# Optimization experiments

Measured on AMD Instinct MI355X. Metric: run time of the kernel, lower is better.

## Reference

```python
import math
import jax, jax.numpy as jnp
import numpy as np

NUM_EXPERTS = 64
HIDDEN = 2048
BATCH, SEQ = 8, 2048


def setup_inputs() -> dict:
    key = jax.random.key(0)
    k1, k2 = jax.random.split(key)
    hidden_states = jax.random.normal(k1, (BATCH, SEQ, HIDDEN), dtype=jnp.float32)
    classifier_weight = jax.random.normal(k2, (HIDDEN, NUM_EXPERTS), dtype=jnp.float32) * (1.0 / math.sqrt(HIDDEN))
    return {"hidden_states": hidden_states, "classifier_weight": classifier_weight}


def _route_tokens(router_logits):
    # router_logits: (tokens, experts). second_expert_policy='all',
    # normalize_router_prob_before_dropping=False, batch_prioritized_routing=True,
    # training mode -> capacity = 2*ceil(tokens/experts), no padding mask.
    n_tokens, n_experts = router_logits.shape
    router_probs = jax.nn.softmax(router_logits, axis=-1)  # router_dtype=float32

    top_1_idx = jnp.argmax(router_probs, axis=-1)
    top_1_mask = jax.nn.one_hot(top_1_idx, n_experts, dtype=router_probs.dtype)
    logits_except_top_1 = jnp.where(top_1_mask > 0, -jnp.inf, router_logits)
    top_2_idx = jnp.argmax(logits_except_top_1, axis=-1)
    top_2_mask = jax.nn.one_hot(top_2_idx, n_experts, dtype=router_probs.dtype)

    # batch-prioritized routing: sort tokens by -max prob, cumsum positions per expert
    importance = -jnp.max(router_probs, axis=-1)  # (tokens,)
    order = jnp.argsort(importance)
    inv_order = jnp.argsort(order)
    sorted_1 = top_1_mask[order]
    locations1 = ((jnp.cumsum(sorted_1, axis=0) - 1.0) * sorted_1)[inv_order]
    sorted_2 = top_2_mask[order]
    locations2 = ((jnp.cumsum(sorted_2, axis=0) - 1.0) * sorted_2)[inv_order]
    locations2 = locations2 + jnp.sum(top_1_mask, axis=0, keepdims=True)

    expert_capacity = 2 * math.ceil(n_tokens / n_experts)  # training path, expert_capacity=None
    top_1_mask = top_1_mask * (locations1 < expert_capacity).astype(top_1_mask.dtype)
    top_2_mask = top_2_mask * (locations2 < expert_capacity).astype(top_2_mask.dtype)

    # normalize AFTER dropping (normalize_router_prob_before_dropping=False)
    top_1_max_probs = jnp.sum(router_probs * top_1_mask, axis=-1)
    top_2_max_probs = jnp.sum(router_probs * top_2_mask, axis=-1)
    denom = jnp.clip(top_1_max_probs + top_2_max_probs, jnp.finfo(router_probs.dtype).eps, None)
    gates1 = (top_1_max_probs / denom)[:, None] * top_1_mask
    gates2 = (top_2_max_probs / denom)[:, None] * top_2_mask
    return top_1_mask, gates1 + gates2


def reference(hidden_states, classifier_weight):
    b, s, h = hidden_states.shape
    x = hidden_states.reshape(b * s, h)
    router_logits = x @ classifier_weight  # (tokens, experts), bias=False
    top_1_mask, router_probs = _route_tokens(router_logits)
    return top_1_mask, router_probs
```

## Files before the change

kernel.cpp:

```cpp
#include <hip/hip_runtime.h>
#include <math.h>

#define TOKENS      16384
#define HID         2048
#define EXPERTS     64
#define CAPSLOT     1024
#define CAP         512

__device__ __forceinline__ void fma8(float* a, float s, float4 w0, float4 w1) {
    a[0] = fmaf(s, w0.x, a[0]); a[1] = fmaf(s, w0.y, a[1]);
    a[2] = fmaf(s, w0.z, a[2]); a[3] = fmaf(s, w0.w, a[3]);
    a[4] = fmaf(s, w1.x, a[4]); a[5] = fmaf(s, w1.y, a[5]);
    a[6] = fmaf(s, w1.z, a[6]); a[7] = fmaf(s, w1.w, a[7]);
}

__global__ __launch_bounds__(256, 2) void k_partial16(
    const float* __restrict__ x, const float* __restrict__ W,
    float* __restrict__ partial, int* __restrict__ cnts)
{
    __shared__ float wl[128 * EXPERTS];

    const int tid = threadIdx.x;
    const int tb = blockIdx.x & 31;
    const int kc = blockIdx.x >> 5;
    const int k0 = kc * 128;

    if (blockIdx.x == 0) {
        for (int i = tid; i < 128 * 16; i += 256) cnts[i] = 0;
    }

    {
        const float4* src = (const float4*)(W + (size_t)k0 * EXPERTS);
        float4* dst = (float4*)wl;
        #pragma unroll
        for (int i = 0; i < 8; ++i)
            dst[i * 256 + tid] = src[i * 256 + tid];
    }
    __syncthreads();

    const int lane = tid & 63;
    const int wv   = tid >> 6;
    const int tg   = lane >> 3;
    const int eg   = lane & 7;
    const int tok0 = tb * 512 + wv * 128 + tg * 16;
    const float* xb = x + (size_t)tok0 * HID + k0;

    float acc[16][8];
    #pragma unroll
    for (int i = 0; i < 16; ++i)
        #pragma unroll
        for (int e = 0; e < 8; ++e) acc[i][e] = 0.f;

    #pragma unroll 1
    for (int k4 = 0; k4 < 128; k4 += 4) {
        float4 xv[16];
        #pragma unroll
        for (int i = 0; i < 16; ++i)
            xv[i] = *(const float4*)(xb + (size_t)i * HID + k4);

        float4 w0[4], w1[4];
        #pragma unroll
        for (int kk = 0; kk < 4; ++kk) {
            const float* wp = &wl[(k4 + kk) * EXPERTS + eg * 8];
            w0[kk] = *(const float4*)wp;
            w1[kk] = *(const float4*)(wp + 4);
        }

        #pragma unroll
        for (int i = 0; i < 16; ++i) {
            fma8(acc[i], xv[i].x, w0[0], w1[0]);
            fma8(acc[i], xv[i].y, w0[1], w1[1]);
            fma8(acc[i], xv[i].z, w0[2], w1[2]);
            fma8(acc[i], xv[i].w, w0[3], w1[3]);
        }
    }

    float* pb = partial + ((size_t)kc * TOKENS + tok0) * EXPERTS + eg * 8;
    #pragma unroll
    for (int i = 0; i < 16; ++i) {
        *(float4*)(pb + (size_t)i * EXPERTS) =
            make_float4(acc[i][0], acc[i][1], acc[i][2], acc[i][3]);
        *(float4*)(pb + (size_t)i * EXPERTS + 4) =
            make_float4(acc[i][4], acc[i][5], acc[i][6], acc[i][7]);
    }
}

template<int KCH>
__global__ __launch_bounds__(256) void k_partial8(
    const float* __restrict__ x, const float* __restrict__ W,
    float* __restrict__ partial, int* __restrict__ cnts)
{
    __shared__ float wl[KCH * EXPERTS];

    const int tid = threadIdx.x;
    const int tb = blockIdx.x & 63;
    const int kc = blockIdx.x >> 6;
    const int k0 = kc * KCH;

    if (blockIdx.x == 0) {
        for (int i = tid; i < 128 * 16; i += 256) cnts[i] = 0;
    }

    {
        const float4* src = (const float4*)(W + (size_t)k0 * EXPERTS);
        float4* dst = (float4*)wl;
        #pragma unroll
        for (int i = 0; i < (KCH * EXPERTS / 4) / 256; ++i)
            dst[i * 256 + tid] = src[i * 256 + tid];
    }
    __syncthreads();

    const int lane = tid & 63;
    const int wv   = tid >> 6;
    const int tg   = lane >> 3;
    const int eg   = lane & 7;
    const int tok0 = tb * 256 + wv * 64 + tg * 8;
    const float* xb = x + (size_t)tok0 * HID + k0;

    float acc[8][8];
    #pragma unroll
    for (int i = 0; i < 8; ++i)
        #pragma unroll
        for (int e = 0; e < 8; ++e) acc[i][e] = 0.f;

    float4 xv[8];
    #pragma unroll
    for (int i = 0; i < 8; ++i)
        xv[i] = *(const float4*)(xb + (size_t)i * HID);

    #pragma unroll 2
    for (int k4 = 0; k4 < KCH; k4 += 4) {
        float4 xn[8];
        const bool more = (k4 + 4 < KCH);
        if (more) {
            #pragma unroll
            for (int i = 0; i < 8; ++i)
                xn[i] = *(const float4*)(xb + (size_t)i * HID + k4 + 4);
        }

        float4 w0[4], w1[4];
        #pragma unroll
        for (int kk = 0; kk < 4; ++kk) {
            const float* wp = &wl[(k4 + kk) * EXPERTS + eg * 8];
            w0[kk] = *(const float4*)wp;
            w1[kk] = *(const float4*)(wp + 4);
        }

        #pragma unroll
        for (int i = 0; i < 8; ++i) {
            fma8(acc[i], xv[i].x, w0[0], w1[0]);
            fma8(acc[i], xv[i].y, w0[1], w1[1]);
            fma8(acc[i], xv[i].z, w0[2], w1[2]);
            fma8(acc[i], xv[i].w, w0[3], w1[3]);
        }

        if (more) {
            #pragma unroll
            for (int i = 0; i < 8; ++i) xv[i] = xn[i];
        }
    }

    float* pb = partial + ((size_t)kc * TOKENS + tok0) * EXPERTS + eg * 8;
    #pragma unroll
    for (int i = 0; i < 8; ++i) {
        *(float4*)(pb + (size_t)i * EXPERTS) =
            make_float4(acc[i][0], acc[i][1], acc[i][2], acc[i][3]);
        *(float4*)(pb + (size_t)i * EXPERTS + 4) =
            make_float4(acc[i][4], acc[i][5], acc[i][6], acc[i][7]);
    }
}

template<int KSPLIT>
__global__ __launch_bounds__(256) void k_route(
    const float* __restrict__ partial,
    float* __restrict__ p1o, float* __restrict__ p2o,
    int* __restrict__ top1o, int* __restrict__ top2o,
    int* __restrict__ cnts, float* __restrict__ bkey, int* __restrict__ btok)
{
    const int tid   = threadIdx.x;
    const int e     = tid & 63;
    const int token = blockIdx.x * 4 + (tid >> 6);

    float logit = 0.f;
    #pragma unroll
    for (int c = 0; c < KSPLIT; ++c)
        logit += partial[((size_t)c * TOKENS + token) * EXPERTS + e];

    float bv = logit; int be = e;
    #pragma unroll
    for (int m = 32; m >= 1; m >>= 1) {
        float ov = __shfl_xor(bv, m);
        int   oe = __shfl_xor(be, m);
        if (ov > bv || (ov == bv && oe < be)) { bv = ov; be = oe; }
    }
    const float m1 = bv;
    const int   e1 = be;

    float bv2 = (e == e1) ? -INFINITY : logit;
    int   be2 = (e == e1) ? (1 << 30) : e;
    #pragma unroll
    for (int m = 32; m >= 1; m >>= 1) {
        float ov = __shfl_xor(bv2, m);
        int   oe = __shfl_xor(be2, m);
        if (ov > bv2 || (ov == bv2 && oe < be2)) { bv2 = ov; be2 = oe; }
    }
    const int e2 = be2;

    float s = expf(logit - m1);
    #pragma unroll
    for (int m = 32; m >= 1; m >>= 1) s += __shfl_xor(s, m);

    if (e == 0) {
        const float P1 = 1.0f / s;
        p1o[token]   = P1;
        p2o[token]   = expf(bv2 - m1) / s;
        top1o[token] = e1;
        top2o[token] = e2;

        int s1 = atomicAdd(&cnts[e1 * 16], 1);
        if (s1 < CAPSLOT) {
            bkey[(size_t)e1 * CAPSLOT + s1] = P1;
            btok[(size_t)e1 * CAPSLOT + s1] = token;
        }
        int s2 = atomicAdd(&cnts[(64 + e2) * 16], 1);
        if (s2 < CAPSLOT) {
            bkey[(size_t)(64 + e2) * CAPSLOT + s2] = P1;
            btok[(size_t)(64 + e2) * CAPSLOT + s2] = token;
        }
    }
}

__global__ __launch_bounds__(256) void k_rank(
    const int* __restrict__ cnts,
    const float* __restrict__ bkey, const int* __restrict__ btok,
    int* __restrict__ keep1, int* __restrict__ keep2)
{
    __shared__ float skey[CAPSLOT];
    __shared__ int   stok[CAPSLOT];

    const int b    = blockIdx.x;
    const int mode = b >> 6;
    const int e    = b & 63;
    const int tid  = threadIdx.x;

    const int n_raw = cnts[b * 16];
    const int n     = min(n_raw, CAPSLOT);
    const int base  = mode ? cnts[e * 16] : 0;

    for (int i = tid; i < n; i += 256) {
        skey[i] = bkey[(size_t)b * CAPSLOT + i];
        stok[i] = btok[(size_t)b * CAPSLOT + i];
    }
    __syncthreads();

    int* __restrict__ keep = mode ? keep2 : keep1;
    for (int i = tid; i < n; i += 256) {
        const float ki = skey[i];
        const int   ti = stok[i];
        int r = base;
        for (int j = 0; j < n; ++j)
            r += (skey[j] > ki || (skey[j] == ki && stok[j] < ti)) ? 1 : 0;
        keep[ti] = (r < CAP) ? 1 : 0;
    }
}

__global__ __launch_bounds__(256) void k_out(
    const float* __restrict__ p1, const float* __restrict__ p2,
    const int* __restrict__ top1, const int* __restrict__ top2,
    const int* __restrict__ keep1, const int* __restrict__ keep2,
    float* __restrict__ out)
{
    const int tid   = threadIdx.x;
    const int token = blockIdx.x * 16 + (tid >> 4);
    const int eb    = (tid & 15) * 4;

    const int  k1 = keep1[token];
    const int  k2 = keep2[token];
    const float P1 = k1 ? p1[token] : 0.0f;
    const float P2 = k2 ? p2[token] : 0.0f;
    const float denom = fmaxf(P1 + P2, 1.1920929e-07f);
    const float g1 = P1 / denom;
    const float g2 = P2 / denom;
    const int e1 = top1[token];
    const int e2 = top2[token];

    float4 mv, pv;
    mv.x = (k1 && e1 == eb + 0) ? 1.0f : 0.0f;
    mv.y = (k1 && e1 == eb + 1) ? 1.0f : 0.0f;
    mv.z = (k1 && e1 == eb + 2) ? 1.0f : 0.0f;
    mv.w = (k1 && e1 == eb + 3) ? 1.0f : 0.0f;
    pv.x = (k1 && e1 == eb + 0) ? g1 : ((k2 && e2 == eb + 0) ? g2 : 0.0f);
    pv.y = (k1 && e1 == eb + 1) ? g1 : ((k2 && e2 == eb + 1) ? g2 : 0.0f);
    pv.z = (k1 && e1 == eb + 2) ? g1 : ((k2 && e2 == eb + 2) ? g2 : 0.0f);
    pv.w = (k1 && e1 == eb + 3) ? g1 : ((k2 && e2 == eb + 3) ? g2 : 0.0f);

    *(float4*)(out + (size_t)token * EXPERTS + eb) = mv;
    *(float4*)(out + (size_t)TOKENS * EXPERTS + (size_t)token * EXPERTS + eb) = pv;
}

extern "C" void kernel_launch(void* const* d_in, const int* in_sizes, int n_in,
                              void* d_out, int out_size, void* d_ws, size_t ws_size,
                              hipStream_t stream)
{
    const float* x = (const float*)d_in[0];
    const float* W = (const float*)d_in[1];
    float* out = (float*)d_out;

    const size_t extras_f = 6 * (size_t)TOKENS + 128 * 16
                          + 2 * 128 * (size_t)CAPSLOT;
    const size_t need16 = ((size_t)16 * TOKENS * EXPERTS + extras_f) * 4;
    const size_t need8  = ((size_t)8  * TOKENS * EXPERTS + extras_f) * 4;

    int ks;
    if (ws_size == 0 || ws_size >= need16) ks = 16;
    else if (ws_size >= need8)             ks = 8;
    else                                   ks = 4;

    float* partial = (float*)d_ws;
    float* p1    = partial + (size_t)ks * TOKENS * EXPERTS;
    float* p2    = p1 + TOKENS;
    int*   top1  = (int*)(p2 + TOKENS);
    int*   top2  = top1 + TOKENS;
    int*   keep1 = top2 + TOKENS;
    int*   keep2 = keep1 + TOKENS;
    int*   cnts  = keep2 + TOKENS;
    float* bkey  = (float*)(cnts + 128 * 16);
    int*   btok  = (int*)(bkey + 128 * CAPSLOT);

    if (ks == 16) {
        k_partial16<<<32 * 16, 256, 0, stream>>>(x, W, partial, cnts);
        k_route<16><<<TOKENS / 4, 256, 0, stream>>>(
            partial, p1, p2, top1, top2, cnts, bkey, btok);
    } else if (ks == 8) {
        k_partial8<256><<<64 * 8, 256, 0, stream>>>(x, W, partial, cnts);
        k_route<8><<<TOKENS / 4, 256, 0, stream>>>(
            partial, p1, p2, top1, top2, cnts, bkey, btok);
    } else {
        k_partial8<512><<<64 * 4, 256, 0, stream>>>(x, W, partial, cnts);
        k_route<4><<<TOKENS / 4, 256, 0, stream>>>(
            partial, p1, p2, top1, top2, cnts, bkey, btok);
    }
    k_rank<<<2 * EXPERTS, 256, 0, stream>>>(cnts, bkey, btok, keep1, keep2);
    k_out<<<TOKENS / 16, 256, 0, stream>>>(
        p1, p2, top1, top2, keep1, keep2, out);
}
```

Measured before the change: 281.8 us.

## Halve per-thread token tile and prefetch next x slice in partial GEMM

The split-K partial GEMM now has each thread compute 8 tokens instead of 16, which halves the accumulator registers and raises the launch-bounds occupancy target from 2 to 4 blocks per CU. The launch uses twice as many blocks. The next float4 slice of x is loaded before the FMAs on the current slice, a register double buffer meant to hide global load latency. In exchange, each shared-memory weight load is reused across fewer tokens and more blocks each reload the weight chunk.

```diff
diff --git a/kernel.cpp b/kernel.cpp
--- a/kernel.cpp
+++ b/kernel.cpp
@@ -14,16 +14,17 @@
     a[6] = fmaf(s, w1.z, a[6]); a[7] = fmaf(s, w1.w, a[7]);
 }
 
-__global__ __launch_bounds__(256, 2) void k_partial16(
+template<int KCH, int TBS>
+__global__ __launch_bounds__(256, 4) void k_partial8(
     const float* __restrict__ x, const float* __restrict__ W,
     float* __restrict__ partial, int* __restrict__ cnts)
 {
-    __shared__ float wl[128 * EXPERTS];
+    __shared__ float wl[KCH * EXPERTS];
 
     const int tid = threadIdx.x;
-    const int tb = blockIdx.x & 31;
-    const int kc = blockIdx.x >> 5;
-    const int k0 = kc * 128;
+    const int tb = blockIdx.x & (TBS - 1);
+    const int kc = blockIdx.x / TBS;
+    const int k0 = kc * KCH;
 
     if (blockIdx.x == 0) {
         for (int i = tid; i < 128 * 16; i += 256) cnts[i] = 0;
@@ -33,7 +34,7 @@
         const float4* src = (const float4*)(W + (size_t)k0 * EXPERTS);
         float4* dst = (float4*)wl;
         #pragma unroll
-        for (int i = 0; i < 8; ++i)
+        for (int i = 0; i < (KCH * EXPERTS / 4) / 256; ++i)
             dst[i * 256 + tid] = src[i * 256 + tid];
     }
     __syncthreads();
@@ -42,21 +43,29 @@
     const int wv   = tid >> 6;
     const int tg   = lane >> 3;
     const int eg   = lane & 7;
-    const int tok0 = tb * 512 + wv * 128 + tg * 16;
+    const int tok0 = tb * 256 + wv * 64 + tg * 8;
     const float* xb = x + (size_t)tok0 * HID + k0;
 
-    float acc[16][8];
-    #pragma unroll
-    for (int i = 0; i < 16; ++i)
+    float acc[8][8];
+    #pragma unroll
+    for (int i = 0; i < 8; ++i)
         #pragma unroll
         for (int e = 0; e < 8; ++e) acc[i][e] = 0.f;
 
-    #pragma unroll 1
-    for (int k4 = 0; k4 < 128; k4 += 4) {
-        float4 xv[16];
-        #pragma unroll
-        for (int i = 0; i < 16; ++i)
-            xv[i] = *(const float4*)(xb + (size_t)i * HID + k4);
+    float4 xv[8];
+    #pragma unroll
+    for (int i = 0; i < 8; ++i)
+        xv[i] = *(const float4*)(xb + (size_t)i * HID);
+
+    #pragma unroll 2
+    for (int k4 = 0; k4 < KCH; k4 += 4) {
+        float4 xn[8];
+        const bool more = (k4 + 4 < KCH);
+        if (more) {
+            #pragma unroll
+            for (int i = 0; i < 8; ++i)
+                xn[i] = *(const float4*)(xb + (size_t)i * HID + k4 + 4);
+        }
 
         float4 w0[4], w1[4];
         #pragma unroll
@@ -67,17 +76,22 @@
         }
 
         #pragma unroll
-        for (int i = 0; i < 16; ++i) {
+        for (int i = 0; i < 8; ++i) {
             fma8(acc[i], xv[i].x, w0[0], w1[0]);
             fma8(acc[i], xv[i].y, w0[1], w1[1]);
             fma8(acc[i], xv[i].z, w0[2], w1[2]);
             fma8(acc[i], xv[i].w, w0[3], w1[3]);
         }
+
+        if (more) {
+            #pragma unroll
+            for (int i = 0; i < 8; ++i) xv[i] = xn[i];
+        }
     }
 
     float* pb = partial + ((size_t)kc * TOKENS + tok0) * EXPERTS + eg * 8;
     #pragma unroll
-    for (int i = 0; i < 16; ++i) {
+    for (int i = 0; i < 8; ++i) {
         *(float4*)(pb + (size_t)i * EXPERTS) =
             make_float4(acc[i][0], acc[i][1], acc[i][2], acc[i][3]);
         *(float4*)(pb + (size_t)i * EXPERTS + 4) =
@@ -86,7 +100,7 @@
 }
 
 template<int KCH>
-__global__ __launch_bounds__(256) void k_partial8(
+__global__ __launch_bounds__(256) void k_partial8lo(
     const float* __restrict__ x, const float* __restrict__ W,
     float* __restrict__ partial, int* __restrict__ cnts)
 {
@@ -328,15 +342,15 @@
     int*   btok  = (int*)(bkey + 128 * CAPSLOT);
 
     if (ks == 16) {
-        k_partial16<<<32 * 16, 256, 0, stream>>>(x, W, partial, cnts);
+        k_partial8<128, 64><<<64 * 16, 256, 0, stream>>>(x, W, partial, cnts);
         k_route<16><<<TOKENS / 4, 256, 0, stream>>>(
             partial, p1, p2, top1, top2, cnts, bkey, btok);
     } else if (ks == 8) {
-        k_partial8<256><<<64 * 8, 256, 0, stream>>>(x, W, partial, cnts);
+        k_partial8lo<256><<<64 * 8, 256, 0, stream>>>(x, W, partial, cnts);
         k_route<8><<<TOKENS / 4, 256, 0, stream>>>(
             partial, p1, p2, top1, top2, cnts, bkey, btok);
     } else {
-        k_partial8<512><<<64 * 4, 256, 0, stream>>>(x, W, partial, cnts);
+        k_partial8lo<512><<<64 * 4, 256, 0, stream>>>(x, W, partial, cnts);
         k_route<4><<<TOKENS / 4, 256, 0, stream>>>(
             partial, p1, p2, top1, top2, cnts, bkey, btok);
     }
```

Result: slower. 1.028 ms (+264.9%).
